# Performance work log

Measured on AMD Instinct MI355X. Metric: run time of the kernel, lower is better.

## Reference

```python
import jax, jax.numpy as jnp
import numpy as np

N_HEAD = 16
N_EMBD = 1024
HEAD_DIM = N_EMBD // N_HEAD
ROPE_BASE = 10000.0


def _rope_tables(T, dim):
    inv_freq = 1.0 / (ROPE_BASE ** (jnp.arange(0, dim, 2, dtype=jnp.float32) / dim))
    t = jnp.arange(T, dtype=jnp.float32)
    freqs = jnp.einsum('i,j->ij', t, inv_freq)          # [T, dim/2]
    emb = jnp.concatenate((freqs, freqs), axis=-1)       # [T, dim]
    return jnp.cos(emb), jnp.sin(emb)


def _rotate_half(x):
    x1, x2 = jnp.split(x, 2, axis=-1)
    return jnp.concatenate((-x2, x1), axis=-1)


def setup_inputs() -> dict:
    key = jax.random.key(0)
    k_x, k_wa, k_ba, k_wp, k_bp = jax.random.split(key, 5)
    B, T, C = 2, 2048, N_EMBD
    x = jax.random.normal(k_x, (B, T, C), dtype=jnp.float32)
    # torch Linear weights: [out, in]
    W_attn = jax.random.normal(k_wa, (3 * C, C), dtype=jnp.float32) * (1.0 / np.sqrt(C))
    b_attn = jax.random.normal(k_ba, (3 * C,), dtype=jnp.float32) * 0.01
    W_proj = jax.random.normal(k_wp, (C, C), dtype=jnp.float32) * (1.0 / np.sqrt(C))
    b_proj = jax.random.normal(k_bp, (C,), dtype=jnp.float32) * 0.01
    return {"x": x, "W_attn": W_attn, "b_attn": b_attn, "W_proj": W_proj, "b_proj": b_proj}


def reference(x, W_attn, b_attn, W_proj, b_proj):
    B, T, C = x.shape
    H, D = N_HEAD, HEAD_DIM
    qkv = jnp.einsum('btc,oc->bto', x, W_attn) + b_attn   # [B,T,3C]
    q, k, v = jnp.split(qkv, 3, axis=2)
    # [B,T,C] -> [B,H,T,D]
    q = q.reshape(B, T, H, D).transpose(0, 2, 1, 3)
    k = k.reshape(B, T, H, D).transpose(0, 2, 1, 3)
    v = v.reshape(B, T, H, D).transpose(0, 2, 1, 3)
    cos, sin = _rope_tables(T, D)                          # [T,D]
    q = q * cos + _rotate_half(q) * sin
    k = k * cos + _rotate_half(k) * sin
    att = jnp.einsum('bhqd,bhkd->bhqk', q, k) * (1.0 / np.sqrt(D))
    causal = jnp.tril(jnp.ones((T, T), dtype=bool))
    att = jnp.where(causal, att, -jnp.inf)
    att = jax.nn.softmax(att, axis=-1)
    y = jnp.einsum('bhqk,bhkd->bhqd', att, v)              # [B,H,T,D]
    y = y.transpose(0, 2, 1, 3).reshape(B, T, C)
    y = jnp.einsum('btc,oc->bto', y, W_proj) + b_proj
    return y
```

## Files before the change

### kernel.cpp

```cpp
#include <hip/hip_runtime.h>


typedef unsigned short u16;
typedef u16 u16x4 __attribute__((ext_vector_type(4)));
typedef u16 u16x8 __attribute__((ext_vector_type(8)));
typedef short s16x8 __attribute__((ext_vector_type(8)));
typedef float f32x4 __attribute__((ext_vector_type(4)));

#define T_SEQ 2048
#define C_EMB 1024
#define NH 16
#define HD 64

#define MFMA16(a, b, c) __builtin_amdgcn_mfma_f32_16x16x32_bf16(a, b, c, 0, 0, 0)

__device__ __forceinline__ u16 f2bf(float f) {
    union { float f; unsigned int i; } x; x.f = f;
    unsigned int r = x.i + 0x7fffu + ((x.i >> 16) & 1u);
    return (u16)(r >> 16);
}
__device__ __forceinline__ u16x4 pack4(f32x4 v) {
    u16x4 o;
#pragma unroll
    for (int j = 0; j < 4; ++j) o[j] = f2bf(v[j]);
    return o;
}

__global__ __launch_bounds__(256) void conv_k(const float* __restrict__ src, u16* __restrict__ dst, int n8) {
    int i = blockIdx.x * 256 + threadIdx.x;
    if (i >= n8) return;
    f32x4 a = ((const f32x4*)src)[i * 2];
    f32x4 b = ((const f32x4*)src)[i * 2 + 1];
    u16x8 o;
#pragma unroll
    for (int j = 0; j < 4; ++j) o[j] = f2bf(a[j]);
#pragma unroll
    for (int j = 0; j < 4; ++j) o[4 + j] = f2bf(b[j]);
    ((u16x8*)dst)[i] = o;
}

__global__ __launch_bounds__(256) void rope_tab_k(float2* __restrict__ tab) {
    int idx = blockIdx.x * 256 + threadIdx.x;
    int t = idx >> 5, j = idx & 31;
    float inv = __builtin_exp2f(-0.41524101186092f * (float)j);
    float s_, c_;
    sincosf((float)t * inv, &s_, &c_);
    tab[idx] = make_float2(c_, s_);
}

__global__ __launch_bounds__(256) void qkv_rope_k(const u16* __restrict__ xb, const u16* __restrict__ Wab,
                                                  const float* __restrict__ bias,
                                                  const float2* __restrict__ tab,
                                                  u16* __restrict__ qb, u16* __restrict__ kb,
                                                  u16* __restrict__ vt) {
    __shared__ u16 smem[2 * 128 * 72];
    u16* As = smem;
    u16* Bs = smem + 128 * 72;
    int tid = threadIdx.x;
    int n0 = blockIdx.x * 128, m0 = blockIdx.y * 128;
    int w = tid >> 6, lane = tid & 63, lr = lane & 15, quad = lane >> 4;
    int wr = w >> 1, wc = w & 1;
    f32x4 acc[4][4] = {};
    for (int kt = 0; kt < C_EMB; kt += 64) {
#pragma unroll
        for (int it = 0; it < 4; ++it) {
            int idx = it * 256 + tid;
            int row = idx >> 3, c8 = (idx & 7) << 3;
            *(s16x8*)&As[row * 72 + c8] = *(const s16x8*)(xb + (size_t)(m0 + row) * C_EMB + kt + c8);
            *(s16x8*)&Bs[row * 72 + c8] = *(const s16x8*)(Wab + (size_t)(n0 + row) * C_EMB + kt + c8);
        }
        __syncthreads();
#pragma unroll
        for (int ks = 0; ks < 64; ks += 32) {
            s16x8 af[4], bf[4];
#pragma unroll
            for (int i = 0; i < 4; ++i)
                af[i] = *(const s16x8*)&As[(wr * 64 + i * 16 + lr) * 72 + ks + quad * 8];
#pragma unroll
            for (int j = 0; j < 4; ++j)
                bf[j] = *(const s16x8*)&Bs[(wc * 64 + j * 16 + lr) * 72 + ks + quad * 8];
#pragma unroll
            for (int i = 0; i < 4; ++i)
#pragma unroll
                for (int j = 0; j < 4; ++j) acc[i][j] = MFMA16(af[i], bf[j], acc[i][j]);
        }
        __syncthreads();
    }
    int sec = n0 >> 10;
    float bv[4];
#pragma unroll
    for (int j = 0; j < 4; ++j) bv[j] = bias[n0 + wc * 64 + j * 16 + lr];

    int h0 = (n0 & 1023) >> 6;
    int b = m0 >> 11, tbase = m0 & 2047;
    if (sec == 2) {
        u16* Ct = smem;
#pragma unroll
        for (int i = 0; i < 4; ++i)
#pragma unroll
            for (int j = 0; j < 4; ++j) {
                f32x4 vv;
#pragma unroll
                for (int r = 0; r < 4; ++r) vv[r] = acc[i][j][r] + bv[j];
                int d = wc * 64 + j * 16 + lr;
                int m4 = wr * 64 + i * 16 + quad * 4;
                *(u16x4*)&Ct[d * 136 + m4] = pack4(vv);
            }
        __syncthreads();
        size_t hb = (size_t)(b * NH);
#pragma unroll
        for (int p = 0; p < 8; ++p) {
            int idx = p * 256 + tid;
            int d = idx >> 4, mc = (idx & 15) << 3;
            s16x8 vdat = *(const s16x8*)&Ct[d * 136 + mc];
            int h = h0 + (d >> 6), dd = d & 63;
            *(s16x8*)(vt + ((hb + h) * HD + dd) * T_SEQ + tbase + mc) = vdat;
        }
    } else {
        u16* dst = (sec == 0) ? qb : kb;
        float qs = (sec == 0) ? 0.18033688011112043f : 1.0f;
        u16* Ct = smem;
#pragma unroll
        for (int i = 0; i < 4; ++i)
#pragma unroll
            for (int r = 0; r < 4; ++r) {
                int mrow = wr * 64 + i * 16 + quad * 4 + r;
                int t = (m0 + mrow) & 2047;
#pragma unroll
                for (int j = 0; j < 2; ++j) {
                    int d1 = j * 16 + lr;
                    float2 cs = tab[t * 32 + d1];
                    float v1 = acc[i][j][r] + bv[j];
                    float v2 = acc[i][j + 2][r] + bv[j + 2];
                    int n1 = wc * 64 + j * 16 + lr;
                    Ct[mrow * 136 + n1]      = f2bf((v1 * cs.x - v2 * cs.y) * qs);
                    Ct[mrow * 136 + n1 + 32] = f2bf((v2 * cs.x + v1 * cs.y) * qs);
                }
            }
        __syncthreads();
#pragma unroll
        for (int p = 0; p < 8; ++p) {
            int idx = p * 256 + tid;
            int mrow = idx >> 4, c = idx & 15;
            s16x8 vdat = *(const s16x8*)&Ct[mrow * 136 + c * 8];
            int h = h0 + (c >> 3), dd = (c & 7) << 3;
            *(s16x8*)(dst + ((size_t)(b * NH + h) * T_SEQ + tbase + mrow) * HD + dd) = vdat;
        }
    }
}

__global__ __launch_bounds__(512, 4) void flash_k(const u16* __restrict__ qb, const u16* __restrict__ kb,
                                                  const u16* __restrict__ vt, u16* __restrict__ yab) {
    __shared__ u16 Ks[2][64 * 72];
    __shared__ u16 Vs[2][64 * 72];
    __shared__ u16 Ps[8][16 * 72];
    int tid = threadIdx.x;
    int bx = blockIdx.x, by = blockIdx.y;
    int qt = (by < 16) ? (15 - bx) : bx;
    int bh = by;
    int w = tid >> 6, lane = tid & 63, lr = lane & 15, quad = lane >> 4;
    int q0 = qt * 128;
    const u16* qh = qb + (size_t)bh * T_SEQ * HD;
    const u16* kh = kb + (size_t)bh * T_SEQ * HD;
    const u16* vh = vt + (size_t)bh * HD * T_SEQ;

    int rbase = q0 + w * 16;

    s16x8 aq[2];
#pragma unroll
    for (int ks = 0; ks < 2; ++ks)
        aq[ks] = *(const s16x8*)(qh + (size_t)(rbase + lr) * HD + ks * 32 + quad * 8);

    int srow = tid >> 3, sc8 = (tid & 7) << 3;

    float m_i = -1e30f, l_i = 0.f;
    f32x4 oacc[4] = {};

    int ktmax = 2 * qt + 1;
    {
        s16x8 kr0 = *(const s16x8*)(kh + (size_t)srow * HD + sc8);
        s16x8 vr0 = *(const s16x8*)(vh + (size_t)srow * T_SEQ + sc8);
        *(s16x8*)&Ks[0][srow * 72 + sc8] = kr0;
        *(s16x8*)&Vs[0][srow * 72 + sc8] = vr0;
    }
    __syncthreads();

    for (int kt = 0; kt <= ktmax; ++kt) {
        int cur = kt & 1;
        int k0 = kt * 64;
        bool pf = kt < ktmax;
        s16x8 kr0, vr0;
        if (pf) {
            int kn = k0 + 64;
            kr0 = *(const s16x8*)(kh + (size_t)(kn + srow) * HD + sc8);
            vr0 = *(const s16x8*)(vh + (size_t)srow * T_SEQ + kn + sc8);
        }
        const u16* Kc = Ks[cur];
        const u16* Vc = Vs[cur];

        if (k0 <= rbase + 15) {
            s16x8 ak[2][4], av[2][4];
#pragma unroll
            for (int ks = 0; ks < 2; ++ks)
#pragma unroll
                for (int tc = 0; tc < 4; ++tc) {
                    ak[ks][tc] = *(const s16x8*)&Kc[(tc * 16 + lr) * 72 + ks * 32 + quad * 8];
                    av[ks][tc] = *(const s16x8*)&Vc[(tc * 16 + lr) * 72 + ks * 32 + quad * 8];
                }
            f32x4 sacc[4] = {};
#pragma unroll
            for (int ks = 0; ks < 2; ++ks)
#pragma unroll
                for (int tc = 0; tc < 4; ++tc) sacc[tc] = MFMA16(ak[ks][tc], aq[ks], sacc[tc]);
            if (k0 + 63 > rbase) {
#pragma unroll
                for (int tc = 0; tc < 4; ++tc)
#pragma unroll
                    for (int r = 0; r < 4; ++r)
                        if (k0 + tc * 16 + quad * 4 + r > rbase + lr) sacc[tc][r] = -1e30f;
            }
            f32x4 mv = sacc[0];
#pragma unroll
            for (int tc = 1; tc < 4; ++tc)
#pragma unroll
                for (int r = 0; r < 4; ++r) mv[r] = fmaxf(mv[r], sacc[tc][r]);
            float mx = fmaxf(fmaxf(mv[0], mv[1]), fmaxf(mv[2], mv[3]));
            mx = fmaxf(mx, __shfl_xor(mx, 16, 64));
            mx = fmaxf(mx, __shfl_xor(mx, 32, 64));
            float mo = m_i;
            bool need = !__all(mx <= mo + 8.0f);
            float alpha = 1.0f;
            if (need) {
                float mn = fmaxf(mo, mx);
                alpha = __builtin_exp2f(mo - mn);
                m_i = mn;
                l_i *= alpha;
            }
            float mnow = m_i;
            f32x4 rv = {0.f, 0.f, 0.f, 0.f};
#pragma unroll
            for (int tc = 0; tc < 4; ++tc)
#pragma unroll
                for (int r = 0; r < 4; ++r) {
                    float p = __builtin_exp2f(sacc[tc][r] - mnow);
                    sacc[tc][r] = p;
                    rv[r] += p;
                }
            float rs = (rv[0] + rv[1]) + (rv[2] + rv[3]);
            rs += __shfl_xor(rs, 16, 64);
            rs += __shfl_xor(rs, 32, 64);
            l_i += rs;
#pragma unroll
            for (int tc = 0; tc < 4; ++tc)
                *(u16x4*)&Ps[w][lr * 72 + tc * 16 + quad * 4] = pack4(sacc[tc]);
            if (need) {
#pragma unroll
                for (int tn = 0; tn < 4; ++tn)
#pragma unroll
                    for (int r = 0; r < 4; ++r) oacc[tn][r] *= alpha;
            }
#pragma unroll
            for (int ks = 0; ks < 2; ++ks) {
                s16x8 ap = *(const s16x8*)&Ps[w][lr * 72 + ks * 32 + quad * 8];
#pragma unroll
                for (int tn = 0; tn < 4; ++tn) oacc[tn] = MFMA16(av[ks][tn], ap, oacc[tn]);
            }
        }
        if (pf) {
            int nx = cur ^ 1;
            *(s16x8*)&Ks[nx][srow * 72 + sc8] = kr0;
            *(s16x8*)&Vs[nx][srow * 72 + sc8] = vr0;
        }
        __syncthreads();
    }
    int b = bh >> 4, hh = bh & 15;
    {
        float inv = 1.f / l_i;
        int t = rbase + lr;
        size_t base = ((size_t)b * T_SEQ + t) * C_EMB + hh * HD;
#pragma unroll
        for (int tn = 0; tn < 4; ++tn) {
            f32x4 vv;
#pragma unroll
            for (int r = 0; r < 4; ++r) vv[r] = oacc[tn][r] * inv;
            *(u16x4*)(yab + base + tn * 16 + quad * 4) = pack4(vv);
        }
    }
}

__global__ __launch_bounds__(256) void proj_k(const u16* __restrict__ ya, const u16* __restrict__ Wpb,
                                              const float* __restrict__ bias, float* __restrict__ out) {
    __shared__ u16 As[128 * 72];
    __shared__ u16 Bs[128 * 72];
    int tid = threadIdx.x;
    int n0 = blockIdx.x * 128, m0 = blockIdx.y * 128;
    int w = tid >> 6, lane = tid & 63, lr = lane & 15, quad = lane >> 4;
    int wr = w >> 1, wc = w & 1;
    f32x4 acc[4][4] = {};
    for (int kt = 0; kt < C_EMB; kt += 64) {
#pragma unroll
        for (int it = 0; it < 4; ++it) {
            int idx = it * 256 + tid;
            int row = idx >> 3, c8 = (idx & 7) << 3;
            *(s16x8*)&As[row * 72 + c8] = *(const s16x8*)(ya + (size_t)(m0 + row) * C_EMB + kt + c8);
            *(s16x8*)&Bs[row * 72 + c8] = *(const s16x8*)(Wpb + (size_t)(n0 + row) * C_EMB + kt + c8);
        }
        __syncthreads();
#pragma unroll
        for (int ks = 0; ks < 64; ks += 32) {
            s16x8 af[4], bf[4];
#pragma unroll
            for (int i = 0; i < 4; ++i)
                af[i] = *(const s16x8*)&As[(wr * 64 + i * 16 + lr) * 72 + ks + quad * 8];
#pragma unroll
            for (int j = 0; j < 4; ++j)
                bf[j] = *(const s16x8*)&Bs[(wc * 64 + j * 16 + lr) * 72 + ks + quad * 8];
#pragma unroll
            for (int i = 0; i < 4; ++i)
#pragma unroll
                for (int j = 0; j < 4; ++j) acc[i][j] = MFMA16(af[i], bf[j], acc[i][j]);
        }
        __syncthreads();
    }
    float bv[4];
#pragma unroll
    for (int j = 0; j < 4; ++j) bv[j] = bias[n0 + wc * 64 + j * 16 + lr];
#pragma unroll
    for (int i = 0; i < 4; ++i)
#pragma unroll
        for (int r = 0; r < 4; ++r) {
            int m = m0 + wr * 64 + i * 16 + quad * 4 + r;
#pragma unroll
            for (int j = 0; j < 4; ++j)
                out[(size_t)m * C_EMB + n0 + wc * 64 + j * 16 + lr] = acc[i][j][r] + bv[j];
        }
}

extern "C" void kernel_launch(void* const* d_in, const int* in_sizes, int n_in,
                              void* d_out, int out_size, void* d_ws, size_t ws_size,
                              hipStream_t stream) {
    const float *x = nullptr, *Wa = nullptr, *ba = nullptr, *Wp = nullptr, *bp = nullptr;
    for (int i = 0; i < n_in; ++i) {
        switch (in_sizes[i]) {
            case 4194304: x  = (const float*)d_in[i]; break;
            case 3145728: Wa = (const float*)d_in[i]; break;
            case 3072:    ba = (const float*)d_in[i]; break;
            case 1048576: Wp = (const float*)d_in[i]; break;
            case 1024:    bp = (const float*)d_in[i]; break;
            default: break;
        }
    }
    float* out = (float*)d_out;

    char* ws = (char*)d_ws;
    u16* qb     = (u16*)(ws);
    u16* kb     = (u16*)(ws + 8388608);
    u16* vt     = (u16*)(ws + 16777216);
    u16* yab    = (u16*)(ws + 25165824);
    float2* tab = (float2*)(ws + 33554432);
    u16* xb     = (u16*)(ws + 35651584);
    u16* Wab    = (u16*)(ws + 44040192);
    u16* Wpb    = (u16*)(ws + 50331648);

    conv_k<<<2048, 256, 0, stream>>>(x, xb, 524288);
    conv_k<<<1536, 256, 0, stream>>>(Wa, Wab, 393216);
    conv_k<<<512, 256, 0, stream>>>(Wp, Wpb, 131072);
    rope_tab_k<<<256, 256, 0, stream>>>(tab);
    qkv_rope_k<<<dim3(24, 32), 256, 0, stream>>>(xb, Wab, ba, tab, qb, kb, vt);
    flash_k<<<dim3(16, 32), 512, 0, stream>>>(qb, kb, vt, yab);
    proj_k<<<dim3(8, 32), 256, 0, stream>>>(yab, Wpb, bp, out);
}
```

Measured before the change: 212.4 us.

## Use direct global-to-LDS loads in GEMMs and defer softmax row-sum reduction

Both GEMM kernels now stage tiles with global_load_lds (16-byte direct-to-LDS loads) instead of register round-trips. This forces an unpadded 64-element row stride, which may add LDS bank conflicts on the MFMA fragment reads. In attention, the per-tile row-sum shuffles are dropped: each lane keeps partial sums, and one reduction runs at the end. The max shuffle now only runs when a rescale is needed, and P is packed with the hardware v_cvt_pk_bf16_f32 instruction.

Measured after the change: 214.4 us. No clear change (+0.9%).

```diff
diff --git a/kernel.cpp b/kernel.cpp
--- a/kernel.cpp
+++ b/kernel.cpp
@@ -24,6 +24,17 @@
 #pragma unroll
     for (int j = 0; j < 4; ++j) o[j] = f2bf(v[j]);
     return o;
+}
+__device__ __forceinline__ u16x4 pack4cvt(f32x4 v) {
+    union { u16x4 h; unsigned int w[2]; } u;
+    asm("v_cvt_pk_bf16_f32 %0, %1, %2" : "=v"(u.w[0]) : "v"(v[0]), "v"(v[1]));
+    asm("v_cvt_pk_bf16_f32 %0, %1, %2" : "=v"(u.w[1]) : "v"(v[2]), "v"(v[3]));
+    return u.h;
+}
+__device__ __forceinline__ void gload16(const void* g, void* l) {
+    __builtin_amdgcn_global_load_lds(
+        (const __attribute__((address_space(1))) unsigned int*)g,
+        (__attribute__((address_space(3))) unsigned int*)l, 16, 0, 0);
 }
 
 __global__ __launch_bounds__(256) void conv_k(const float* __restrict__ src, u16* __restrict__ dst, int n8) {
@@ -53,21 +64,22 @@
                                                   const float2* __restrict__ tab,
                                                   u16* __restrict__ qb, u16* __restrict__ kb,
                                                   u16* __restrict__ vt) {
-    __shared__ u16 smem[2 * 128 * 72];
+    __shared__ u16 smem[17408];
     u16* As = smem;
-    u16* Bs = smem + 128 * 72;
+    u16* Bs = smem + 8192;
     int tid = threadIdx.x;
     int n0 = blockIdx.x * 128, m0 = blockIdx.y * 128;
     int w = tid >> 6, lane = tid & 63, lr = lane & 15, quad = lane >> 4;
     int wr = w >> 1, wc = w & 1;
     f32x4 acc[4][4] = {};
+    int srow = tid >> 3, sc8 = (tid & 7) << 3;
     for (int kt = 0; kt < C_EMB; kt += 64) {
 #pragma unroll
         for (int it = 0; it < 4; ++it) {
-            int idx = it * 256 + tid;
-            int row = idx >> 3, c8 = (idx & 7) << 3;
-            *(s16x8*)&As[row * 72 + c8] = *(const s16x8*)(xb + (size_t)(m0 + row) * C_EMB + kt + c8);
-            *(s16x8*)&Bs[row * 72 + c8] = *(const s16x8*)(Wab + (size_t)(n0 + row) * C_EMB + kt + c8);
+            int row = it * 32 + srow;
+            int off = (it * 256 + tid) * 8;
+            gload16(xb + (size_t)(m0 + row) * C_EMB + kt + sc8, &As[off]);
+            gload16(Wab + (size_t)(n0 + row) * C_EMB + kt + sc8, &Bs[off]);
         }
         __syncthreads();
 #pragma unroll
@@ -75,10 +87,10 @@
             s16x8 af[4], bf[4];
 #pragma unroll
             for (int i = 0; i < 4; ++i)
-                af[i] = *(const s16x8*)&As[(wr * 64 + i * 16 + lr) * 72 + ks + quad * 8];
+                af[i] = *(const s16x8*)&As[(wr * 64 + i * 16 + lr) * 64 + ks + quad * 8];
 #pragma unroll
             for (int j = 0; j < 4; ++j)
-                bf[j] = *(const s16x8*)&Bs[(wc * 64 + j * 16 + lr) * 72 + ks + quad * 8];
+                bf[j] = *(const s16x8*)&Bs[(wc * 64 + j * 16 + lr) * 64 + ks + quad * 8];
 #pragma unroll
             for (int i = 0; i < 4; ++i)
 #pragma unroll
@@ -173,7 +185,8 @@
 
     int srow = tid >> 3, sc8 = (tid & 7) << 3;
 
-    float m_i = -1e30f, l_i = 0.f;
+    float m_i = -1e30f;
+    f32x4 l4 = {0.f, 0.f, 0.f, 0.f};
     f32x4 oacc[4] = {};
 
     int ktmax = 2 * qt + 1;
@@ -224,35 +237,30 @@
             for (int tc = 1; tc < 4; ++tc)
 #pragma unroll
                 for (int r = 0; r < 4; ++r) mv[r] = fmaxf(mv[r], sacc[tc][r]);
-            float mx = fmaxf(fmaxf(mv[0], mv[1]), fmaxf(mv[2], mv[3]));
-            mx = fmaxf(mx, __shfl_xor(mx, 16, 64));
-            mx = fmaxf(mx, __shfl_xor(mx, 32, 64));
-            float mo = m_i;
-            bool need = !__all(mx <= mo + 8.0f);
+            float loc = fmaxf(fmaxf(mv[0], mv[1]), fmaxf(mv[2], mv[3]));
+            bool need = !__all(loc <= m_i + 8.0f);
             float alpha = 1.0f;
             if (need) {
-                float mn = fmaxf(mo, mx);
-                alpha = __builtin_exp2f(mo - mn);
+                float mx = fmaxf(loc, __shfl_xor(loc, 16, 64));
+                mx = fmaxf(mx, __shfl_xor(mx, 32, 64));
+                float mn = fmaxf(m_i, mx);
+                alpha = __builtin_exp2f(m_i - mn);
                 m_i = mn;
-                l_i *= alpha;
+#pragma unroll
+                for (int r = 0; r < 4; ++r) l4[r] *= alpha;
             }
             float mnow = m_i;
-            f32x4 rv = {0.f, 0.f, 0.f, 0.f};
 #pragma unroll
             for (int tc = 0; tc < 4; ++tc)
 #pragma unroll
                 for (int r = 0; r < 4; ++r) {
                     float p = __builtin_exp2f(sacc[tc][r] - mnow);
                     sacc[tc][r] = p;
-                    rv[r] += p;
+                    l4[r] += p;
                 }
-            float rs = (rv[0] + rv[1]) + (rv[2] + rv[3]);
-            rs += __shfl_xor(rs, 16, 64);
-            rs += __shfl_xor(rs, 32, 64);
-            l_i += rs;
 #pragma unroll
             for (int tc = 0; tc < 4; ++tc)
-                *(u16x4*)&Ps[w][lr * 72 + tc * 16 + quad * 4] = pack4(sacc[tc]);
+                *(u16x4*)&Ps[w][lr * 72 + tc * 16 + quad * 4] = pack4cvt(sacc[tc]);
             if (need) {
 #pragma unroll
                 for (int tn = 0; tn < 4; ++tn)
@@ -273,9 +281,12 @@
         }
         __syncthreads();
     }
+    float rs = (l4[0] + l4[1]) + (l4[2] + l4[3]);
+    rs += __shfl_xor(rs, 16, 64);
+    rs += __shfl_xor(rs, 32, 64);
     int b = bh >> 4, hh = bh & 15;
     {
-        float inv = 1.f / l_i;
+        float inv = 1.f / rs;
         int t = rbase + lr;
         size_t base = ((size_t)b * T_SEQ + t) * C_EMB + hh * HD;
 #pragma unroll
@@ -290,20 +301,21 @@
 
 __global__ __launch_bounds__(256) void proj_k(const u16* __restrict__ ya, const u16* __restrict__ Wpb,
                                               const float* __restrict__ bias, float* __restrict__ out) {
-    __shared__ u16 As[128 * 72];
-    __shared__ u16 Bs[128 * 72];
+    __shared__ u16 As[8192];
+    __shared__ u16 Bs[8192];
     int tid = threadIdx.x;
     int n0 = blockIdx.x * 128, m0 = blockIdx.y * 128;
     int w = tid >> 6, lane = tid & 63, lr = lane & 15, quad = lane >> 4;
     int wr = w >> 1, wc = w & 1;
     f32x4 acc[4][4] = {};
+    int srow = tid >> 3, sc8 = (tid & 7) << 3;
     for (int kt = 0; kt < C_EMB; kt += 64) {
 #pragma unroll
         for (int it = 0; it < 4; ++it) {
-            int idx = it * 256 + tid;
-            int row = idx >> 3, c8 = (idx & 7) << 3;
-            *(s16x8*)&As[row * 72 + c8] = *(const s16x8*)(ya + (size_t)(m0 + row) * C_EMB + kt + c8);
-            *(s16x8*)&Bs[row * 72 + c8] = *(const s16x8*)(Wpb + (size_t)(n0 + row) * C_EMB + kt + c8);
+            int row = it * 32 + srow;
+            int off = (it * 256 + tid) * 8;
+            gload16(ya + (size_t)(m0 + row) * C_EMB + kt + sc8, &As[off]);
+            gload16(Wpb + (size_t)(n0 + row) * C_EMB + kt + sc8, &Bs[off]);
         }
         __syncthreads();
 #pragma unroll
@@ -311,10 +323,10 @@
             s16x8 af[4], bf[4];
 #pragma unroll
             for (int i = 0; i < 4; ++i)
-                af[i] = *(const s16x8*)&As[(wr * 64 + i * 16 + lr) * 72 + ks + quad * 8];
+                af[i] = *(const s16x8*)&As[(wr * 64 + i * 16 + lr) * 64 + ks + quad * 8];
 #pragma unroll
             for (int j = 0; j < 4; ++j)
-                bf[j] = *(const s16x8*)&Bs[(wc * 64 + j * 16 + lr) * 72 + ks + quad * 8];
+                bf[j] = *(const s16x8*)&Bs[(wc * 64 + j * 16 + lr) * 64 + ks + quad * 8];
 #pragma unroll
             for (int i = 0; i < 4; ++i)
 #pragma unroll
```
